# Kernel tuning notes

Hardware: AMD Instinct MI355X
Metric: run time of the kernel (lower is better)

The kernel has to match this reference:

```python
import jax, jax.numpy as jnp
import numpy as np

B, T, C_IN, HID, WIN = 16384, 20, 256, 256, 3


def tb_mask(T=20, win=3):
    # Faithful replica of TemporalCrossAttent.TB (including its quirky indexing).
    m = np.zeros((T, T), dtype=np.float32)
    for i in range(T):
        if i - win < 0:
            m[i, :win] = 1
        elif i + win >= T:
            m[i, T - win:] = 1
        else:
            m[i - win // 2, i - win // 2:i + win // 2] = 1
    return jnp.asarray(np.where(m == 1, 0.0, -1e22).astype(np.float32))


def setup_inputs() -> dict:
    key = jax.random.key(0)
    k1, k2, k3, k4, k5 = jax.random.split(key, 5)
    scale = 0.05  # xavier-ish init scale for 256x256
    return {
        "feat1": jax.random.normal(k1, (B, T, C_IN), dtype=jnp.float32),
        "feat2": jax.random.normal(k2, (B, T, C_IN), dtype=jnp.float32),
        "Wq": jax.random.normal(k3, (HID, C_IN), dtype=jnp.float32) * scale,
        "Wk": jax.random.normal(k4, (HID, C_IN), dtype=jnp.float32) * scale,
        "Wv": jax.random.normal(k5, (HID, C_IN), dtype=jnp.float32) * scale,
    }


def reference(feat1, feat2, Wq, Wk, Wv):
    # Conv1d(kernel_size=1, bias=False) == pointwise linear over channels.
    mask = tb_mask(T, WIN)  # [T, T] static banded additive mask
    q = jnp.einsum('btc,hc->bth', feat1, Wq)  # [B,T,HID]
    k = jnp.einsum('btc,hc->bth', feat2, Wk)
    v = jnp.einsum('btc,hc->bth', feat2, Wv)
    sim = jnp.einsum('bth,bsh->bts', q, k) / jnp.sqrt(jnp.float32(HID))
    attn = jax.nn.softmax(sim + mask, axis=-1)  # [B,T,T]
    # dropout layers act as identity in eval mode
    return jnp.einsum('bts,bsh->bth', attn, v)  # [B,T,HID]
```

## Files before the change

kernel.cpp:

```cpp
#include <hip/hip_runtime.h>
#include <stdint.h>

#define NBATCH 16384
#define TT     20
#define CC     256
#define FP     260
#define LDK    264
#define TP     40
#define NT     512
#define BPB    64

typedef __bf16 bf16x8 __attribute__((ext_vector_type(8)));
typedef float  f32x4  __attribute__((ext_vector_type(4)));

#define GLL16(g, l) __builtin_amdgcn_global_load_lds( \
    (const __attribute__((address_space(1))) uint32_t*)(g), \
    (__attribute__((address_space(3))) uint32_t*)(l), 16, 0, 0)

#define BAR_LGKM() do { asm volatile("s_waitcnt lgkmcnt(0)" ::: "memory"); \
                        __builtin_amdgcn_s_barrier(); } while (0)
#define BAR_VM0()  do { asm volatile("s_waitcnt vmcnt(0) lgkmcnt(0)" ::: "memory"); \
                        __builtin_amdgcn_s_barrier(); } while (0)

__constant__ int8_t c_CNT[TT] = {3,3,4,2,2,2,2,2,2,2,2,2,2,2,2,2,0,3,3,3};
__constant__ int8_t c_OFF[TT] = {0,3,6,10,12,14,16,18,20,22,24,26,28,30,32,34,0,36,39,42};
__constant__ int8_t c_PT[45]  = {0,0,0,1,1,1,2,2,2,2,3,3,4,4,5,5,6,6,7,7,8,8,9,9,
                                 10,10,11,11,12,12,13,13,14,14,15,15,17,17,17,18,18,18,19,19,19};
__constant__ int8_t c_PS[45]  = {0,1,2,0,1,2,0,1,2,3,3,4,4,5,5,6,6,7,7,8,8,9,9,10,
                                 10,11,11,12,12,13,13,14,14,15,15,16,17,18,19,17,18,19,17,18,19};

__device__ __forceinline__ uint16_t f2bf(float f) {
    __bf16 b = (__bf16)f;
    return __builtin_bit_cast(uint16_t, b);
}
__device__ __forceinline__ uint32_t pk2(float a, float b) {
    return (uint32_t)f2bf(a) | ((uint32_t)f2bf(b) << 16);
}
__device__ __forceinline__ float bflo(uint32_t u) { return __builtin_bit_cast(float, u << 16); }
__device__ __forceinline__ float bfhi(uint32_t u) { return __builtin_bit_cast(float, u & 0xffff0000u); }

__global__ void prep1_kernel(const float* __restrict__ Wq, const float* __restrict__ Wk,
                             const float* __restrict__ Wv, uint16_t* __restrict__ mqkT,
                             uint16_t* __restrict__ wvb) {
    const int n = blockIdx.x;
    const int k = threadIdx.x;
    float acc = 0.f;
    for (int h = 0; h < CC; ++h)
        acc = fmaf(Wk[h * CC + n], Wq[h * CC + k], acc);
    mqkT[n * CC + k] = f2bf(acc * 0.0625f);
    wvb[n * CC + k]  = f2bf(Wv[n * CC + k]);
}

__global__ void prep2_kernel(const uint16_t* __restrict__ mqkT, const uint16_t* __restrict__ wvb,
                             uint16_t* __restrict__ BqS, uint16_t* __restrict__ BvS) {
    const int bid = blockIdx.x;
    const int m  = bid >> 6;
    const int w  = (bid >> 3) & 7;
    const int kk = bid & 7;
    const int mt   = threadIdx.x >> 6;
    const int lane = threadIdx.x & 63;
    const uint16_t* src = m ? wvb : mqkT;
    uint16_t*       dst = m ? BvS : BqS;
    const int n   = w * 32 + mt * 16 + (lane & 15);
    const int col = kk * 32 + ((lane >> 4) << 3);
    uint4 v = *(const uint4*)(src + n * CC + col);
    *(uint4*)(dst + ((size_t)((w * 16 + kk * 2 + mt) * 64 + lane) << 3)) = v;
}

__device__ __forceinline__ bf16x8 ldsAf(const float* __restrict__ sF, int r, int u) {
    const float* p = sF + r * FP + (u << 3);
    float4 lo = *(const float4*)p;
    float4 hi = *(const float4*)(p + 4);
    uint4 q;
    q.x = pk2(lo.x, lo.y); q.y = pk2(lo.z, lo.w);
    q.z = pk2(hi.x, hi.y); q.w = pk2(hi.z, hi.w);
    return __builtin_bit_cast(bf16x8, q);
}

__global__ __launch_bounds__(NT, 2)
void attn_main(const float* __restrict__ f1g, const float* __restrict__ f2g,
               const uint16_t* __restrict__ BqS, const uint16_t* __restrict__ BvS,
               float* __restrict__ outg) {
    __shared__ float    sF1[2][TT * FP];
    __shared__ float    sF2[2][TT * FP];
    __shared__ uint16_t sT [TT * LDK];
    __shared__ uint16_t sVT[256 * TP];
    __shared__ uint16_t attnL[32 * 32];
    __shared__ float    s_simE[45];

    const int tid  = threadIdx.x;
    const int lane = tid & 63;
    const int w    = tid >> 6;
    const int l15  = lane & 15;
    const int q    = lane >> 4;
    const size_t blockBase = (size_t)blockIdx.x * BPB * TT * CC;

    bf16x8 Bq[2][8], Bv[2][8];
#pragma unroll
    for (int kk = 0; kk < 8; ++kk)
#pragma unroll
        for (int mt = 0; mt < 2; ++mt) {
            const size_t idx = ((size_t)((w * 16 + kk * 2 + mt) * 64 + lane)) << 3;
            Bq[mt][kk] = __builtin_bit_cast(bf16x8, *(const uint4*)(BqS + idx));
            Bv[mt][kk] = __builtin_bit_cast(bf16x8, *(const uint4*)(BvS + idx));
        }

    const float* srcTen = (w < 4 ? f1g : f2g) + blockBase;
    const int rw = (w & 3) * 5;

#pragma unroll
    for (int j = 0; j < 5; ++j) {
        int r = rw + j;
        GLL16(srcTen + r * 256 + (lane << 2), (w < 4 ? sF1[0] : sF2[0]) + r * FP);
    }
    {
        uint32_t* aL = (uint32_t*)attnL;
        aL[tid] = ((tid >> 4) == 16 && (tid & 15) < 10) ? 0x3F803F80u : 0u;
    }
    BAR_VM0();

    const int rB0 = l15;
    const int rB1 = (16 + l15 < TT) ? 16 + l15 : TT - 1;

    for (int i = 0; i < BPB; ++i) {
        const int cur = i & 1, nxt = cur ^ 1;

        if (i + 1 < BPB) {
            const float* sp = srcTen + (size_t)(i + 1) * TT * CC;
            float* dp = (w < 4 ? sF1[nxt] : sF2[nxt]);
#pragma unroll
            for (int j = 0; j < 5; ++j) {
                int r = rw + j;
                GLL16(sp + r * 256 + (lane << 2), dp + r * FP);
            }
        }
        const float* F1 = sF1[cur];
        const float* F2 = sF2[cur];

        {
            f32x4 acc[2][2];
#pragma unroll
            for (int mt = 0; mt < 2; ++mt)
#pragma unroll
                for (int ct = 0; ct < 2; ++ct)
                    acc[mt][ct] = f32x4{0.f, 0.f, 0.f, 0.f};
#pragma unroll
            for (int kk = 0; kk < 8; ++kk) {
                const int u = (kk << 2) + q;
                bf16x8 b0 = ldsAf(F1, rB0, u);
                bf16x8 b1 = ldsAf(F1, rB1, u);
#pragma unroll
                for (int mt = 0; mt < 2; ++mt) {
                    acc[mt][0] = __builtin_amdgcn_mfma_f32_16x16x32_bf16(Bq[mt][kk], b0, acc[mt][0], 0, 0, 0);
                    acc[mt][1] = __builtin_amdgcn_mfma_f32_16x16x32_bf16(Bq[mt][kk], b1, acc[mt][1], 0, 0, 0);
                }
            }
#pragma unroll
            for (int mt = 0; mt < 2; ++mt)
#pragma unroll
                for (int ct = 0; ct < 2; ++ct) {
                    int t = ct * 16 + l15;
                    if (t < TT) {
                        int h0 = (w << 5) + mt * 16 + (q << 2);
                        uint2 u2;
                        u2.x = pk2(acc[mt][ct][0], acc[mt][ct][1]);
                        u2.y = pk2(acc[mt][ct][2], acc[mt][ct][3]);
                        *(uint2*)&sT[t * LDK + h0] = u2;
                    }
                }
        }
        BAR_LGKM();

        if (tid < 360) {
            int d = tid >> 3, p = tid & 7;
            int t = c_PT[d], s = c_PS[d];
            const uint16_t* ap = sT + t * LDK + (p << 5);
            const float*    bp = F2 + s * FP + (p << 5);
            float da = 0.f;
#pragma unroll
            for (int jj = 0; jj < 4; ++jj) {
                uint4 ua = *(const uint4*)(ap + (jj << 3));
                float4 lo = *(const float4*)(bp + (jj << 3));
                float4 hi = *(const float4*)(bp + (jj << 3) + 4);
                da = fmaf(bflo(ua.x), lo.x, da);
                da = fmaf(bfhi(ua.x), lo.y, da);
                da = fmaf(bflo(ua.y), lo.z, da);
                da = fmaf(bfhi(ua.y), lo.w, da);
                da = fmaf(bflo(ua.z), hi.x, da);
                da = fmaf(bfhi(ua.z), hi.y, da);
                da = fmaf(bflo(ua.w), hi.z, da);
                da = fmaf(bfhi(ua.w), hi.w, da);
            }
            da += __shfl_xor(da, 1);
            da += __shfl_xor(da, 2);
            da += __shfl_xor(da, 4);
            if (p == 0) {
                float e = __expf(da);
                attnL[t * 32 + s] = f2bf(e);
                s_simE[d] = e;
            }
        }
        {
            f32x4 av[2][2];
#pragma unroll
            for (int rt = 0; rt < 2; ++rt)
#pragma unroll
                for (int ct = 0; ct < 2; ++ct)
                    av[rt][ct] = f32x4{0.f, 0.f, 0.f, 0.f};
#pragma unroll
            for (int kk = 0; kk < 8; ++kk) {
                const int u = (kk << 2) + q;
                bf16x8 a0 = ldsAf(F2, rB0, u);
                bf16x8 a1 = ldsAf(F2, rB1, u);
#pragma unroll
                for (int ct = 0; ct < 2; ++ct) {
                    av[0][ct] = __builtin_amdgcn_mfma_f32_16x16x32_bf16(a0, Bv[ct][kk], av[0][ct], 0, 0, 0);
                    av[1][ct] = __builtin_amdgcn_mfma_f32_16x16x32_bf16(a1, Bv[ct][kk], av[1][ct], 0, 0, 0);
                }
            }
#pragma unroll
            for (int ct = 0; ct < 2; ++ct) {
                int h = (w << 5) + ct * 16 + l15;
                {
                    uint2 u2;
                    u2.x = pk2(av[0][ct][0], av[0][ct][1]);
                    u2.y = pk2(av[0][ct][2], av[0][ct][3]);
                    *(uint2*)&sVT[h * TP + (q << 2)] = u2;
                }
                {
                    uint2 u2;
                    if (q == 0) {
                        u2.x = pk2(av[1][ct][0], av[1][ct][1]);
                        u2.y = pk2(av[1][ct][2], av[1][ct][3]);
                    } else { u2.x = 0u; u2.y = 0u; }
                    *(uint2*)&sVT[h * TP + 16 + (q << 2)] = u2;
                }
            }
        }
        BAR_VM0();

        {
            bf16x8 pa0 = __builtin_bit_cast(bf16x8, *(const uint4*)&attnL[l15 * 32 + (q << 3)]);
            bf16x8 pa1 = __builtin_bit_cast(bf16x8, *(const uint4*)&attnL[(16 + l15) * 32 + (q << 3)]);
            const f32x4 z = f32x4{0.f, 0.f, 0.f, 0.f};
            f32x4 o[2][2];
#pragma unroll
            for (int ct = 0; ct < 2; ++ct) {
                bf16x8 pb = __builtin_bit_cast(bf16x8,
                    *(const uint4*)&sVT[((w << 5) + ct * 16 + l15) * TP + (q << 3)]);
                o[0][ct] = __builtin_amdgcn_mfma_f32_16x16x32_bf16(pa0, pb, z, 0, 0, 0);
                o[1][ct] = __builtin_amdgcn_mfma_f32_16x16x32_bf16(pa1, pb, z, 0, 0, 0);
            }
            const size_t ob = blockBase + (size_t)i * TT * CC;
#pragma unroll
            for (int rt = 0; rt < 2; ++rt)
#pragma unroll
                for (int j = 0; j < 4; ++j) {
                    int t = rt * 16 + (q << 2) + j;
                    if (t < TT) {
                        int cnt = c_CNT[t], off = c_OFF[t];
                        float rs = (cnt == 0) ? 20.0f : s_simE[off];
#pragma unroll
                        for (int jj = 1; jj < 4; ++jj)
                            if (jj < cnt) rs += s_simE[off + jj];
                        float iv = __builtin_amdgcn_rcpf(rs);
                        float* op = outg + ob + (size_t)t * CC + (w << 5) + l15;
                        op[0]  = o[rt][0][j] * iv;
                        op[16] = o[rt][1][j] * iv;
                    }
                }
        }
    }
}

extern "C" void kernel_launch(void* const* d_in, const int* in_sizes, int n_in,
                              void* d_out, int out_size, void* d_ws, size_t ws_size,
                              hipStream_t stream) {
    const float* feat1 = (const float*)d_in[0];
    const float* feat2 = (const float*)d_in[1];
    const float* Wq    = (const float*)d_in[2];
    const float* Wk    = (const float*)d_in[3];
    const float* Wv    = (const float*)d_in[4];
    uint16_t* mqkT = (uint16_t*)d_ws;
    uint16_t* wvb  = mqkT + CC * CC;
    uint16_t* BqS  = wvb  + CC * CC;
    uint16_t* BvS  = BqS  + CC * CC;

    prep1_kernel<<<CC, CC, 0, stream>>>(Wq, Wk, Wv, mqkT, wvb);
    prep2_kernel<<<128, 128, 0, stream>>>(mqkT, wvb, BqS, BvS);
    attn_main<<<NBATCH / BPB, NT, 0, stream>>>(feat1, feat2, BqS, BvS, (float*)d_out);
}
```

Measured before the change: 415.9 us.

## Stream feat1 directly from global, single-buffer feat2 in LDS, reload weights per use

Removes the double-buffered LDS staging of feat1 and instead loads the Q-side operand straight from global memory into registers. feat2 is now single-buffered in a packed shared region, and its prefetch for the next item is issued after the V projection. The preloaded weight fragments are dropped in favour of per-iteration global (cache-resident) loads, and batches per block drop from 64 to 16 (4x more blocks). This cuts LDS footprint and register pressure to allow more occupancy, at the cost of exposed global latency on feat1 and repeated weight loads.

Result: slower. 918.2 us (+120.8%).

```diff
diff --git a/kernel.cpp b/kernel.cpp
--- a/kernel.cpp
+++ b/kernel.cpp
@@ -8,7 +8,7 @@
 #define LDK    264
 #define TP     40
 #define NT     512
-#define BPB    64
+#define BPB    16
 
 typedef __bf16 bf16x8 __attribute__((ext_vector_type(8)));
 typedef float  f32x4  __attribute__((ext_vector_type(4)));
@@ -17,9 +17,9 @@
     (const __attribute__((address_space(1))) uint32_t*)(g), \
     (__attribute__((address_space(3))) uint32_t*)(l), 16, 0, 0)
 
+#define BAR_VM()   do { asm volatile("s_waitcnt vmcnt(0) lgkmcnt(0)" ::: "memory"); \
+                        __builtin_amdgcn_s_barrier(); } while (0)
 #define BAR_LGKM() do { asm volatile("s_waitcnt lgkmcnt(0)" ::: "memory"); \
-                        __builtin_amdgcn_s_barrier(); } while (0)
-#define BAR_VM0()  do { asm volatile("s_waitcnt vmcnt(0) lgkmcnt(0)" ::: "memory"); \
                         __builtin_amdgcn_s_barrier(); } while (0)
 
 __constant__ int8_t c_CNT[TT] = {3,3,4,2,2,2,2,2,2,2,2,2,2,2,2,2,0,3,3,3};
@@ -38,6 +38,13 @@
 }
 __device__ __forceinline__ float bflo(uint32_t u) { return __builtin_bit_cast(float, u << 16); }
 __device__ __forceinline__ float bfhi(uint32_t u) { return __builtin_bit_cast(float, u & 0xffff0000u); }
+
+__device__ __forceinline__ bf16x8 cvt8(float4 x, float4 y) {
+    uint4 q;
+    q.x = pk2(x.x, x.y); q.y = pk2(x.z, x.w);
+    q.z = pk2(y.x, y.y); q.w = pk2(y.z, y.w);
+    return __builtin_bit_cast(bf16x8, q);
+}
 
 __global__ void prep1_kernel(const float* __restrict__ Wq, const float* __restrict__ Wk,
                              const float* __restrict__ Wv, uint16_t* __restrict__ mqkT,
@@ -71,73 +78,55 @@
     const float* p = sF + r * FP + (u << 3);
     float4 lo = *(const float4*)p;
     float4 hi = *(const float4*)(p + 4);
-    uint4 q;
-    q.x = pk2(lo.x, lo.y); q.y = pk2(lo.z, lo.w);
-    q.z = pk2(hi.x, hi.y); q.w = pk2(hi.z, hi.w);
-    return __builtin_bit_cast(bf16x8, q);
+    return cvt8(lo, hi);
 }
 
 __global__ __launch_bounds__(NT, 2)
 void attn_main(const float* __restrict__ f1g, const float* __restrict__ f2g,
                const uint16_t* __restrict__ BqS, const uint16_t* __restrict__ BvS,
                float* __restrict__ outg) {
-    __shared__ float    sF1[2][TT * FP];
-    __shared__ float    sF2[2][TT * FP];
-    __shared__ uint16_t sT [TT * LDK];
-    __shared__ uint16_t sVT[256 * TP];
-    __shared__ uint16_t attnL[32 * 32];
-    __shared__ float    s_simE[45];
+    __shared__ uint16_t smem[26656];
+    float*    f2f    = (float*)smem;
+    uint16_t* attnL  = smem + 10400;
+    float*    s_simE = (float*)(smem + 11040);
+    uint16_t* sT     = smem + 11136;
+    uint16_t* sVT    = smem + 16416;
 
     const int tid  = threadIdx.x;
     const int lane = tid & 63;
     const int w    = tid >> 6;
     const int l15  = lane & 15;
     const int q    = lane >> 4;
-    const size_t blockBase = (size_t)blockIdx.x * BPB * TT * CC;
-
-    bf16x8 Bq[2][8], Bv[2][8];
-#pragma unroll
-    for (int kk = 0; kk < 8; ++kk)
-#pragma unroll
-        for (int mt = 0; mt < 2; ++mt) {
-            const size_t idx = ((size_t)((w * 16 + kk * 2 + mt) * 64 + lane)) << 3;
-            Bq[mt][kk] = __builtin_bit_cast(bf16x8, *(const uint4*)(BqS + idx));
-            Bv[mt][kk] = __builtin_bit_cast(bf16x8, *(const uint4*)(BvS + idx));
-        }
-
-    const float* srcTen = (w < 4 ? f1g : f2g) + blockBase;
-    const int rw = (w & 3) * 5;
-
-#pragma unroll
-    for (int j = 0; j < 5; ++j) {
-        int r = rw + j;
-        GLL16(srcTen + r * 256 + (lane << 2), (w < 4 ? sF1[0] : sF2[0]) + r * FP);
-    }
-    {
-        uint32_t* aL = (uint32_t*)attnL;
-        aL[tid] = ((tid >> 4) == 16 && (tid & 15) < 10) ? 0x3F803F80u : 0u;
-    }
-    BAR_VM0();
+    const size_t bbase = (size_t)blockIdx.x * BPB * TT * CC;
 
     const int rB0 = l15;
     const int rB1 = (16 + l15 < TT) ? 16 + l15 : TT - 1;
 
+    {
+        const float* f2n = f2g + bbase;
+        if (w < 4) {
+#pragma unroll
+            for (int j = 0; j < 3; ++j) {
+                int r = w * 3 + j;
+                GLL16(f2n + r * 256 + (lane << 2), f2f + r * FP);
+            }
+        } else {
+#pragma unroll
+            for (int j = 0; j < 2; ++j) {
+                int r = 12 + (w - 4) * 2 + j;
+                GLL16(f2n + r * 256 + (lane << 2), f2f + r * FP);
+            }
+        }
+        uint32_t* aL = (uint32_t*)attnL;
+        if (tid < 320)
+            aL[tid] = ((tid >> 4) == 16 && (tid & 15) < 10) ? 0x3F803F80u : 0u;
+    }
+
     for (int i = 0; i < BPB; ++i) {
-        const int cur = i & 1, nxt = cur ^ 1;
-
-        if (i + 1 < BPB) {
-            const float* sp = srcTen + (size_t)(i + 1) * TT * CC;
-            float* dp = (w < 4 ? sF1[nxt] : sF2[nxt]);
-#pragma unroll
-            for (int j = 0; j < 5; ++j) {
-                int r = rw + j;
-                GLL16(sp + r * 256 + (lane << 2), dp + r * FP);
-            }
-        }
-        const float* F1 = sF1[cur];
-        const float* F2 = sF2[cur];
+        const bool hasNext = (i + 1 < BPB);
 
         {
+            const float* f1 = f1g + bbase + (size_t)i * TT * CC;
             f32x4 acc[2][2];
 #pragma unroll
             for (int mt = 0; mt < 2; ++mt)
@@ -147,12 +136,16 @@
 #pragma unroll
             for (int kk = 0; kk < 8; ++kk) {
                 const int u = (kk << 2) + q;
-                bf16x8 b0 = ldsAf(F1, rB0, u);
-                bf16x8 b1 = ldsAf(F1, rB1, u);
+                const float* p0 = f1 + rB0 * 256 + (u << 3);
+                const float* p1 = f1 + rB1 * 256 + (u << 3);
+                bf16x8 b0 = cvt8(*(const float4*)p0, *(const float4*)(p0 + 4));
+                bf16x8 b1 = cvt8(*(const float4*)p1, *(const float4*)(p1 + 4));
 #pragma unroll
                 for (int mt = 0; mt < 2; ++mt) {
-                    acc[mt][0] = __builtin_amdgcn_mfma_f32_16x16x32_bf16(Bq[mt][kk], b0, acc[mt][0], 0, 0, 0);
-                    acc[mt][1] = __builtin_amdgcn_mfma_f32_16x16x32_bf16(Bq[mt][kk], b1, acc[mt][1], 0, 0, 0);
+                    bf16x8 am = __builtin_bit_cast(bf16x8,
+                        *(const uint4*)(BqS + ((size_t)((w * 16 + kk * 2 + mt) * 64 + lane) << 3)));
+                    acc[mt][0] = __builtin_amdgcn_mfma_f32_16x16x32_bf16(am, b0, acc[mt][0], 0, 0, 0);
+                    acc[mt][1] = __builtin_amdgcn_mfma_f32_16x16x32_bf16(am, b1, acc[mt][1], 0, 0, 0);
                 }
             }
 #pragma unroll
@@ -169,13 +162,13 @@
                     }
                 }
         }
-        BAR_LGKM();
+        BAR_VM();
 
         if (tid < 360) {
             int d = tid >> 3, p = tid & 7;
             int t = c_PT[d], s = c_PS[d];
             const uint16_t* ap = sT + t * LDK + (p << 5);
-            const float*    bp = F2 + s * FP + (p << 5);
+            const float*    bp = f2f + s * FP + (p << 5);
             float da = 0.f;
 #pragma unroll
             for (int jj = 0; jj < 4; ++jj) {
@@ -210,12 +203,14 @@
 #pragma unroll
             for (int kk = 0; kk < 8; ++kk) {
                 const int u = (kk << 2) + q;
-                bf16x8 a0 = ldsAf(F2, rB0, u);
-                bf16x8 a1 = ldsAf(F2, rB1, u);
+                bf16x8 a0 = ldsAf(f2f, rB0, u);
+                bf16x8 a1 = ldsAf(f2f, rB1, u);
 #pragma unroll
                 for (int ct = 0; ct < 2; ++ct) {
-                    av[0][ct] = __builtin_amdgcn_mfma_f32_16x16x32_bf16(a0, Bv[ct][kk], av[0][ct], 0, 0, 0);
-                    av[1][ct] = __builtin_amdgcn_mfma_f32_16x16x32_bf16(a1, Bv[ct][kk], av[1][ct], 0, 0, 0);
+                    bf16x8 bm = __builtin_bit_cast(bf16x8,
+                        *(const uint4*)(BvS + ((size_t)((w * 16 + kk * 2 + ct) * 64 + lane) << 3)));
+                    av[0][ct] = __builtin_amdgcn_mfma_f32_16x16x32_bf16(a0, bm, av[0][ct], 0, 0, 0);
+                    av[1][ct] = __builtin_amdgcn_mfma_f32_16x16x32_bf16(a1, bm, av[1][ct], 0, 0, 0);
                 }
             }
 #pragma unroll
@@ -237,8 +232,25 @@
                 }
             }
         }
-        BAR_VM0();
-
+        BAR_LGKM();
+
+        if (hasNext) {
+            const float* f2n = f2g + bbase + (size_t)(i + 1) * TT * CC;
+            if (w < 4) {
+#pragma unroll
+                for (int j = 0; j < 3; ++j) {
+                    int r = w * 3 + j;
+                    GLL16(f2n + r * 256 + (lane << 2), f2f + r * FP);
+                }
+            } else {
+#pragma unroll
+                for (int j = 0; j < 2; ++j) {
+                    int r = 12 + (w - 4) * 2 + j;
+                    GLL16(f2n + r * 256 + (lane << 2), f2f + r * FP);
+                }
+            }
+            __builtin_amdgcn_sched_barrier(0);
+        }
         {
             bf16x8 pa0 = __builtin_bit_cast(bf16x8, *(const uint4*)&attnL[l15 * 32 + (q << 3)]);
             bf16x8 pa1 = __builtin_bit_cast(bf16x8, *(const uint4*)&attnL[(16 + l15) * 32 + (q << 3)]);
@@ -251,7 +263,7 @@
                 o[0][ct] = __builtin_amdgcn_mfma_f32_16x16x32_bf16(pa0, pb, z, 0, 0, 0);
                 o[1][ct] = __builtin_amdgcn_mfma_f32_16x16x32_bf16(pa1, pb, z, 0, 0, 0);
             }
-            const size_t ob = blockBase + (size_t)i * TT * CC;
+            const size_t ob = bbase + (size_t)i * TT * CC;
 #pragma unroll
             for (int rt = 0; rt < 2; ++rt)
 #pragma unroll
```
